# Kernel optimization log

Measured on AMD Instinct MI355X. Metric: run time of the kernel, lower is better.

## Reference

```python
import jax, jax.numpy as jnp
import numpy as np

K = 7          # kernel_size
G = 16         # groups
PAD = K // 2   # unfold padding


def setup_inputs() -> dict:
    key = jax.random.key(0)
    ks = jax.random.split(key, 5)
    B, C, H, W = 4, 64, 128, 128
    R = 16  # reduced_chs = _make_divisible(64 * 0.25, 4)
    x = jax.random.normal(ks[0], (B, C, H, W), jnp.float32)
    # ConvBnAct(reduce): 1x1 conv C->R, bias, ReLU (bn=False)
    w_reduce = jax.random.normal(ks[1], (R, C), jnp.float32) * 0.1
    b_reduce = jax.random.normal(ks[2], (R,), jnp.float32) * 0.1
    # span: 1x1 conv R -> K*K*G, bias
    w_span = jax.random.normal(ks[3], (K * K * G, R), jnp.float32) * 0.1
    b_span = jax.random.normal(ks[4], (K * K * G,), jnp.float32) * 0.1
    return dict(x=x, w_reduce=w_reduce, b_reduce=b_reduce,
                w_span=w_span, b_span=b_span)


def reference(x, w_reduce, b_reduce, w_span, b_span):
    B, C, H, W = x.shape
    # kernel-generation branch (stride=1 so no avg-pool)
    red = jax.nn.relu(jnp.einsum('rc,bchw->brhw', w_reduce, x)
                      + b_reduce[None, :, None, None])          # (B,R,H,W)
    kern = (jnp.einsum('or,brhw->bohw', w_span, red)
            + b_span[None, :, None, None])                      # (B,K*K*G,H,W)
    kern = kern.reshape(B, G, K * K, H, W)
    kern = jax.nn.softmax(kern, axis=2)                         # softmax over K*K

    # fused gather-weight-reduce: never materialize the (B,G,C/G,K*K,H,W) unfold
    xp = jnp.pad(x, ((0, 0), (0, 0), (PAD, PAD), (PAD, PAD)))
    xg = xp.reshape(B, G, C // G, H + 2 * PAD, W + 2 * PAD)
    out = jnp.zeros((B, G, C // G, H, W), x.dtype)
    for i in range(K):           # fixed 7x7 taps, unrolled
        for j in range(K):
            # unfold ordering: tap index k = i*K + j (row-major over kernel)
            out = out + kern[:, :, None, i * K + j] * xg[:, :, :, i:i + H, j:j + W]
    return out.reshape(B, C, H, W)
```

## Files before the change

kernel.cpp:

```cpp
#include <hip/hip_runtime.h>

typedef float  f32x4  __attribute__((ext_vector_type(4)));
typedef short  bf16x8 __attribute__((ext_vector_type(8)));

#define KS 7
#define NG 16
#define PAD 3
#define NB 4
#define NC 64
#define NH 128
#define NW 128
#define HW (NH*NW)
#define NR 16
#define CG 4
#define KK 49
#define L2E 1.44269504088896f
#define PADB -100000.0f
#define TS 16
#define HT 22

__device__ __forceinline__ unsigned short bf16rn(float f) {
    unsigned u = __float_as_uint(f);
    u += 0x7FFFu + ((u >> 16) & 1u);
    return (unsigned short)(u >> 16);
}
__device__ __forceinline__ float bf16tof(unsigned short h) {
    return __uint_as_float(((unsigned)h) << 16);
}

__global__ __launch_bounds__(256)
void red_kernel(const float* __restrict__ x,
                const float* __restrict__ w_reduce,
                const float* __restrict__ b_reduce,
                unsigned short* __restrict__ redpk) {
    __shared__ float wT[NC][4];
    const int t  = threadIdx.x;
    const int rq = blockIdx.y;
    { int e = t >> 6, c = t & 63; wT[c][e] = w_reduce[(rq*4+e)*NC + c]; }
    __syncthreads();

    const int pth = blockIdx.x*256 + t;
    const int b   = pth >> 14;
    const int pix = pth & 16383;

    float aa[4];
    #pragma unroll
    for (int i = 0; i < 4; ++i) aa[i] = b_reduce[rq*4+i];

    const float* xp = x + (size_t)b*(NC*HW) + pix;
    #pragma unroll 16
    for (int c = 0; c < NC; ++c) {
        float xv = xp[(size_t)c*HW];
        float4 ww = *(const float4*)&wT[c][0];
        aa[0] = fmaf(ww.x, xv, aa[0]);
        aa[1] = fmaf(ww.y, xv, aa[1]);
        aa[2] = fmaf(ww.z, xv, aa[2]);
        aa[3] = fmaf(ww.w, xv, aa[3]);
    }

    unsigned short hv[4], lv[4];
    #pragma unroll
    for (int i = 0; i < 4; ++i) {
        float sv = fmaxf(aa[i], 0.f) * L2E;
        unsigned short h = bf16rn(sv);
        hv[i] = h;
        lv[i] = bf16rn(sv - bf16tof(h));
    }
    unsigned short* rp = redpk + ((size_t)pth << 5);
    *(ushort4*)(rp + rq*4)      = make_ushort4(hv[0],hv[1],hv[2],hv[3]);
    *(ushort4*)(rp + 16 + rq*4) = make_ushort4(lv[0],lv[1],lv[2],lv[3]);
}

__global__ __launch_bounds__(256, 4)
void invol_kernel(const float* __restrict__ x,
                  const float* __restrict__ w_span,
                  const float* __restrict__ b_span,
                  const unsigned short* __restrict__ redpk,
                  float* __restrict__ out) {
    __shared__ float4 xs[4][HT][HT];

    const int t    = threadIdx.x;
    const int lane = t & 63;
    const int wv   = __builtin_amdgcn_readfirstlane(t >> 6);
    const int p    = lane & 15;
    const int q    = lane >> 4;
    const int h0   = (blockIdx.x >> 3) * TS;
    const int w0   = (blockIdx.x & 7) * TS;
    const int g    = blockIdx.y * 4 + wv;
    const int b    = blockIdx.z;

    const float* xb = x + (size_t)(b*NC + g*CG)*HW;
    #pragma unroll
    for (int it = 0; it < 8; ++it) {
        int idx = lane + it*64;
        if (idx < HT*HT) {
            int hh = idx / HT, ww = idx - hh*HT;
            int gh = h0 + hh - PAD, gw = w0 + ww - PAD;
            float4 v = make_float4(0.f,0.f,0.f,0.f);
            if ((unsigned)gh < NH && (unsigned)gw < NW) {
                const float* pp = xb + gh*NW + gw;
                v.x = pp[0]; v.y = pp[HW]; v.z = pp[2*HW]; v.w = pp[3*HW];
            }
            xs[wv][hh][ww] = v;
        }
    }
    __syncthreads();

    const float* wg = w_span + (size_t)g*(KK*NR);
    bf16x8 A1[4];
    #pragma unroll
    for (int tt = 0; tt < 4; ++tt) {
        int tap = tt*16 + p; if (tap > 48) tap = 48;
        const float4* wr = (const float4*)(wg + tap*NR + (q & 1)*8);
        float4 u0 = wr[0], u1 = wr[1];
        float w8[8] = {u0.x,u0.y,u0.z,u0.w,u1.x,u1.y,u1.z,u1.w};
        bf16x8 a;
        #pragma unroll
        for (int i = 0; i < 8; ++i) {
            unsigned short h = bf16rn(w8[i]);
            unsigned short l = bf16rn(w8[i] - bf16tof(h));
            a[i] = (short)(q < 2 ? h : l);
        }
        A1[tt] = a;
    }

    const float* bg = b_span + g*KK;
    f32x4 bias[4];
    #pragma unroll
    for (int tt = 0; tt < 3; ++tt) {
        float4 bb = *(const float4*)(bg + tt*16 + q*4);
        bias[tt][0] = bb.x*L2E; bias[tt][1] = bb.y*L2E;
        bias[tt][2] = bb.z*L2E; bias[tt][3] = bb.w*L2E;
    }
    bias[3][0] = (q == 0) ? bg[48]*L2E : PADB;
    bias[3][1] = PADB; bias[3][2] = PADB; bias[3][3] = PADB;

    const float4* gp[13];
    #pragma unroll
    for (int tt = 0; tt < 3; ++tt) {
        #pragma unroll
        for (int r = 0; r < 4; ++r) {
            int tap = tt*16 + q*4 + r;
            int i = tap / 7, j = tap - i*7;
            gp[tt*4+r] = &xs[wv][i][p + j];
        }
    }
    gp[12] = &xs[wv][6][p + 6];

    bf16x8 zz;
    #pragma unroll
    for (int i = 0; i < 8; ++i) zz[i] = 0;

    const unsigned short* rb =
        redpk + (((size_t)b*HW + (size_t)h0*NW + w0 + p) << 5) + ((q & 1) << 3);
    bf16x8 B1 = *(const bf16x8*)rb;
    bf16x8 B2 = *(const bf16x8*)(rb + 16);
    B2 = (q < 2) ? B2 : zz;

    #pragma unroll
    for (int ph = 0; ph < TS; ++ph) {
        bf16x8 B1n = B1, B2n = B2;
        if (ph < TS-1) {
            const unsigned short* rn = rb + (size_t)(ph+1)*(NW*32);
            B1n = *(const bf16x8*)rn;
            bf16x8 l2 = *(const bf16x8*)(rn + 16);
            B2n = (q < 2) ? l2 : zz;
        }

        f32x4 ac[4];
        #pragma unroll
        for (int tt = 0; tt < 4; ++tt) {
            f32x4 c0 = __builtin_amdgcn_mfma_f32_16x16x32_bf16(A1[tt], B1, bias[tt], 0,0,0);
            ac[tt]   = __builtin_amdgcn_mfma_f32_16x16x32_bf16(A1[tt], B2, c0,      0,0,0);
        }

        float e[16];
        float sum = 0.f;
        #pragma unroll
        for (int tt = 0; tt < 4; ++tt) {
            #pragma unroll
            for (int r = 0; r < 4; ++r) {
                float ev = exp2f(ac[tt][r]);
                e[tt*4+r] = ev;
                sum += ev;
            }
        }
        sum += __shfl_xor(sum, 16);
        sum += __shfl_xor(sum, 32);

        float g0 = 0.f, g1 = 0.f, g2 = 0.f, g3 = 0.f;
        #pragma unroll
        for (int k = 0; k < 12; ++k) {
            float4 v = gp[k][ph*HT];
            float ev = e[k];
            g0 = fmaf(ev, v.x, g0); g1 = fmaf(ev, v.y, g1);
            g2 = fmaf(ev, v.z, g2); g3 = fmaf(ev, v.w, g3);
        }
        {
            float4 v = gp[12][ph*HT];
            float ev = e[12];
            g0 = fmaf(ev, v.x, g0); g1 = fmaf(ev, v.y, g1);
            g2 = fmaf(ev, v.z, g2); g3 = fmaf(ev, v.w, g3);
        }
        g0 += __shfl_xor(g0, 16); g0 += __shfl_xor(g0, 32);
        g1 += __shfl_xor(g1, 16); g1 += __shfl_xor(g1, 32);
        g2 += __shfl_xor(g2, 16); g2 += __shfl_xor(g2, 32);
        g3 += __shfl_xor(g3, 16); g3 += __shfl_xor(g3, 32);

        if (q == 0) {
            float inv = 1.0f / sum;
            const int h = h0 + ph, w = w0 + p;
            size_t ob = ((size_t)(b*NC + g*CG)*NH + h)*NW + w;
            out[ob]        = g0 * inv;
            out[ob + HW]   = g1 * inv;
            out[ob + 2*HW] = g2 * inv;
            out[ob + 3*HW] = g3 * inv;
        }
        B1 = B1n; B2 = B2n;
    }
}

extern "C" void kernel_launch(void* const* d_in, const int* in_sizes, int n_in,
                              void* d_out, int out_size, void* d_ws, size_t ws_size,
                              hipStream_t stream) {
    const float* x        = (const float*)d_in[0];
    const float* w_reduce = (const float*)d_in[1];
    const float* b_reduce = (const float*)d_in[2];
    const float* w_span   = (const float*)d_in[3];
    const float* b_span   = (const float*)d_in[4];
    float* out = (float*)d_out;
    unsigned short* redpk = (unsigned short*)d_ws;

    red_kernel<<<dim3(NB*HW/256, 4), 256, 0, stream>>>(x, w_reduce, b_reduce, redpk);

    dim3 gridB(64, NG/4, NB);
    invol_kernel<<<gridB, 256, 0, stream>>>(x, w_span, b_span, redpk, out);
}
```

Measured before the change: 55.45 us.

## Store input tile in fp16 LDS, use packed FMA, halve block size

The shared-memory input tile is now stored as half precision (two half2 per pixel), which halves LDS footprint and read bandwidth. The weighted gather uses packed two-wide float FMAs, and only the 13 live exp2 values are computed instead of 16. Blocks shrink to two waves (two groups each) with twice as many blocks, raising occupancy and block count. Rounding x to fp16 adds precision loss on the input values.

```diff
diff --git a/kernel.cpp b/kernel.cpp
--- a/kernel.cpp
+++ b/kernel.cpp
@@ -1,6 +1,8 @@
 #include <hip/hip_runtime.h>
+#include <hip/hip_fp16.h>
 
 typedef float  f32x4  __attribute__((ext_vector_type(4)));
+typedef float  v2f    __attribute__((ext_vector_type(2)));
 typedef short  bf16x8 __attribute__((ext_vector_type(8)));
 
 #define KS 7
@@ -19,6 +21,8 @@
 #define TS 16
 #define HT 22
 
+struct __align__(8) H4 { __half2 ab, cd; };
+
 __device__ __forceinline__ unsigned short bf16rn(float f) {
     unsigned u = __float_as_uint(f);
     u += 0x7FFFu + ((u >> 16) & 1u);
@@ -71,13 +75,13 @@
     *(ushort4*)(rp + 16 + rq*4) = make_ushort4(lv[0],lv[1],lv[2],lv[3]);
 }
 
-__global__ __launch_bounds__(256, 4)
+__global__ __launch_bounds__(128, 4)
 void invol_kernel(const float* __restrict__ x,
                   const float* __restrict__ w_span,
                   const float* __restrict__ b_span,
                   const unsigned short* __restrict__ redpk,
                   float* __restrict__ out) {
-    __shared__ float4 xs[4][HT][HT];
+    __shared__ H4 xs[2][HT][HT];
 
     const int t    = threadIdx.x;
     const int lane = t & 63;
@@ -86,7 +90,7 @@
     const int q    = lane >> 4;
     const int h0   = (blockIdx.x >> 3) * TS;
     const int w0   = (blockIdx.x & 7) * TS;
-    const int g    = blockIdx.y * 4 + wv;
+    const int g    = blockIdx.y * 2 + wv;
     const int b    = blockIdx.z;
 
     const float* xb = x + (size_t)(b*NC + g*CG)*HW;
@@ -101,7 +105,10 @@
                 const float* pp = xb + gh*NW + gw;
                 v.x = pp[0]; v.y = pp[HW]; v.z = pp[2*HW]; v.w = pp[3*HW];
             }
-            xs[wv][hh][ww] = v;
+            H4 hq;
+            hq.ab = __floats2half2_rn(v.x, v.y);
+            hq.cd = __floats2half2_rn(v.z, v.w);
+            xs[wv][hh][ww] = hq;
         }
     }
     __syncthreads();
@@ -135,7 +142,7 @@
     bias[3][0] = (q == 0) ? bg[48]*L2E : PADB;
     bias[3][1] = PADB; bias[3][2] = PADB; bias[3][3] = PADB;
 
-    const float4* gp[13];
+    const H4* gp[13];
     #pragma unroll
     for (int tt = 0; tt < 3; ++tt) {
         #pragma unroll
@@ -174,10 +181,10 @@
             ac[tt]   = __builtin_amdgcn_mfma_f32_16x16x32_bf16(A1[tt], B2, c0,      0,0,0);
         }
 
-        float e[16];
+        float e[13];
         float sum = 0.f;
         #pragma unroll
-        for (int tt = 0; tt < 4; ++tt) {
+        for (int tt = 0; tt < 3; ++tt) {
             #pragma unroll
             for (int r = 0; r < 4; ++r) {
                 float ev = exp2f(ac[tt][r]);
@@ -185,23 +192,22 @@
                 sum += ev;
             }
         }
+        e[12] = exp2f(ac[3][0]);
+        sum += e[12];
         sum += __shfl_xor(sum, 16);
         sum += __shfl_xor(sum, 32);
 
-        float g0 = 0.f, g1 = 0.f, g2 = 0.f, g3 = 0.f;
-        #pragma unroll
-        for (int k = 0; k < 12; ++k) {
-            float4 v = gp[k][ph*HT];
-            float ev = e[k];
-            g0 = fmaf(ev, v.x, g0); g1 = fmaf(ev, v.y, g1);
-            g2 = fmaf(ev, v.z, g2); g3 = fmaf(ev, v.w, g3);
-        }
-        {
-            float4 v = gp[12][ph*HT];
-            float ev = e[12];
-            g0 = fmaf(ev, v.x, g0); g1 = fmaf(ev, v.y, g1);
-            g2 = fmaf(ev, v.z, g2); g3 = fmaf(ev, v.w, g3);
-        }
+        v2f a01 = {0.f, 0.f}, a23 = {0.f, 0.f};
+        #pragma unroll
+        for (int k = 0; k < 13; ++k) {
+            H4 v = gp[k][ph*HT];
+            float2 f01 = __half22float2(v.ab);
+            float2 f23 = __half22float2(v.cd);
+            v2f ee = {e[k], e[k]};
+            a01 += ee * (v2f){f01.x, f01.y};
+            a23 += ee * (v2f){f23.x, f23.y};
+        }
+        float g0 = a01[0], g1 = a01[1], g2 = a23[0], g3 = a23[1];
         g0 += __shfl_xor(g0, 16); g0 += __shfl_xor(g0, 32);
         g1 += __shfl_xor(g1, 16); g1 += __shfl_xor(g1, 32);
         g2 += __shfl_xor(g2, 16); g2 += __shfl_xor(g2, 32);
@@ -233,6 +239,6 @@
 
     red_kernel<<<dim3(NB*HW/256, 4), 256, 0, stream>>>(x, w_reduce, b_reduce, redpk);
 
-    dim3 gridB(64, NG/4, NB);
-    invol_kernel<<<gridB, 256, 0, stream>>>(x, w_span, b_span, redpk, out);
-}
+    dim3 gridB(64, NG/2, NB);
+    invol_kernel<<<gridB, 128, 0, stream>>>(x, w_span, b_span, redpk, out);
+}
```

After: 57.86 us. +4.4%, slower.
